# Kernel tuning notes

Hardware: AMD Instinct MI355X
Metric: run time of the kernel (lower is better)

## Reference

```python
import jax, jax.numpy as jnp
import numpy as np

H = 1024       # hidden_size
I = 1024       # intermediate_size
E = 16         # num_experts
K = 4          # experts_per_token
LIMIT = 7.0    # swiglu_limit
ALPHA = 1.702  # swiglu alpha
EPS = 1e-5     # rmsnorm eps


def setup_inputs() -> dict:
    key = jax.random.key(0)
    ks = jax.random.split(key, 8)
    x = jax.random.normal(ks[0], (2, 512, H), dtype=jnp.float32)
    norm_scale = jnp.ones((H,), dtype=jnp.float32)
    wg = jax.random.normal(ks[1], (H, E), dtype=jnp.float32) * 0.02
    bg = jax.random.normal(ks[2], (E,), dtype=jnp.float32) * 0.02
    w1 = jax.random.normal(ks[3], (E, H, 2 * I), dtype=jnp.float32) * 0.02
    b1 = jax.random.normal(ks[4], (E, 2 * I), dtype=jnp.float32) * 0.02
    w2 = jax.random.normal(ks[5], (E, I, H), dtype=jnp.float32) * 0.02
    b2 = jax.random.normal(ks[6], (E, H), dtype=jnp.float32) * 0.02
    return {"x": x, "norm_scale": norm_scale, "wg": wg, "bg": bg,
            "w1": w1, "b1": b1, "w2": w2, "b2": b2}


def reference(x, norm_scale, wg, bg, w1, b1, w2, b2):
    shape = x.shape
    xf = x.reshape(-1, shape[-1])                                   # [T, H]
    # RMSNorm (float32 math)
    xn = xf * jax.lax.rsqrt(jnp.mean(xf * xf, axis=-1, keepdims=True) + EPS) * norm_scale
    # router logits + top-k with softmax over selected logits
    logits = xn @ wg + bg                                           # [T, E]
    vals, idx = jax.lax.top_k(logits, K)                            # [T, K]
    gates = jax.nn.softmax(vals, axis=-1)                           # [T, K]
    # dense [T, E] gate matrix (exactly equivalent to gather/scatter grouped GEMM)
    gate_full = jnp.einsum('tke,tk->te', jax.nn.one_hot(idx, E, dtype=gates.dtype), gates)
    # expert FFN 1 + fused swiglu (interleaved gate/linear pairs)
    h = jnp.einsum('th,ehd->etd', xn, w1) + b1[:, None, :]          # [E, T, 2I]
    a = jnp.minimum(h[..., ::2], LIMIT)                             # gate branch
    b = jnp.clip(h[..., 1::2], -LIMIT, LIMIT)                       # linear branch
    s = a * jax.nn.sigmoid(ALPHA * a) * (b + 1.0)                   # [E, T, I]
    # expert FFN 2; gamma (gate) scales the full epilogue incl. bias
    y = jnp.einsum('eti,eih->eth', s, w2) + b2[:, None, :]          # [E, T, H]
    t = jnp.einsum('eth,te->th', y, gate_full)                      # scatter-combine
    return x + t.reshape(shape)
```

## Files before the change

kernel.cpp:

```cpp
#include <hip/hip_runtime.h>

#define NH 1024
#define NI2 2048
#define NI 1024
#define NE 16
#define NT 1024

static constexpr float LIMITF = 7.0f;
static constexpr float ALPHAF = 1.702f;
static constexpr float EPSF = 1e-5f;

typedef short bf16x8 __attribute__((ext_vector_type(8)));
typedef float f32x16 __attribute__((ext_vector_type(16)));

__device__ __forceinline__ unsigned short f2bf(float f) {
  unsigned int u = __builtin_bit_cast(unsigned int, f);
  u = (u + 0x7FFFu + ((u >> 16) & 1u)) >> 16;
  return (unsigned short)u;
}

__global__ __launch_bounds__(256) void k_init(const float* __restrict__ x,
                                              float* __restrict__ out) {
  int i = blockIdx.x * 256 + threadIdx.x;
  reinterpret_cast<float4*>(out)[i] = reinterpret_cast<const float4*>(x)[i];
}

__global__ __launch_bounds__(256) void k_norm_router(
    const float* __restrict__ x, const float* __restrict__ nsc,
    const float* __restrict__ wg, const float* __restrict__ bg,
    unsigned short* __restrict__ xn, int* __restrict__ topk_idx,
    float* __restrict__ topk_gate, int* __restrict__ counts) {
  int t = blockIdx.x;
  int tid = threadIdx.x;
  int wave = tid >> 6, lane = tid & 63;

  float4 v = reinterpret_cast<const float4*>(x + (size_t)t * NH)[tid];
  float ss = v.x * v.x + v.y * v.y + v.z * v.z + v.w * v.w;
  for (int off = 32; off; off >>= 1) ss += __shfl_xor(ss, off);

  __shared__ float red[4];
  __shared__ float redl[4][16];
  __shared__ float logits_s[16];
  if (lane == 0) red[wave] = ss;
  __syncthreads();
  float tot = red[0] + red[1] + red[2] + red[3];
  float r = rsqrtf(tot * (1.0f / NH) + EPSF);

  float4 sc = reinterpret_cast<const float4*>(nsc)[tid];
  float xv[4];
  xv[0] = v.x * r * sc.x;
  xv[1] = v.y * r * sc.y;
  xv[2] = v.z * r * sc.z;
  xv[3] = v.w * r * sc.w;

  ushort4 o;
  o.x = f2bf(xv[0]); o.y = f2bf(xv[1]); o.z = f2bf(xv[2]); o.w = f2bf(xv[3]);
  reinterpret_cast<ushort4*>(xn + (size_t)t * NH)[tid] = o;

  float acc[16];
#pragma unroll
  for (int e = 0; e < 16; e++) acc[e] = 0.f;
  int hbase = tid * 4;
#pragma unroll
  for (int i = 0; i < 4; i++) {
    const float4* wr = reinterpret_cast<const float4*>(wg + (size_t)(hbase + i) * NE);
#pragma unroll
    for (int j = 0; j < 4; j++) {
      float4 w = wr[j];
      acc[j * 4 + 0] += xv[i] * w.x;
      acc[j * 4 + 1] += xv[i] * w.y;
      acc[j * 4 + 2] += xv[i] * w.z;
      acc[j * 4 + 3] += xv[i] * w.w;
    }
  }
#pragma unroll
  for (int e = 0; e < 16; e++)
    for (int off = 32; off; off >>= 1) acc[e] += __shfl_xor(acc[e], off);
  if (lane == 0) {
#pragma unroll
    for (int e = 0; e < 16; e++) redl[wave][e] = acc[e];
  }
  __syncthreads();
  if (tid < 16)
    logits_s[tid] = redl[0][tid] + redl[1][tid] + redl[2][tid] + redl[3][tid] + bg[tid];
  __syncthreads();

  if (tid == 0) {
    float vals[16];
#pragma unroll
    for (int e = 0; e < 16; e++) vals[e] = logits_s[e];
    int sel[4]; float sv[4];
    unsigned used = 0;
    for (int k = 0; k < 4; k++) {
      float best = -1e30f; int bi = 0;
      for (int e = 0; e < 16; e++) {
        if (!((used >> e) & 1u) && vals[e] > best) { best = vals[e]; bi = e; }
      }
      used |= 1u << bi; sel[k] = bi; sv[k] = best;
    }
    float g[4], ssum = 0.f;
    for (int k = 0; k < 4; k++) { g[k] = __expf(sv[k] - sv[0]); ssum += g[k]; }
    for (int k = 0; k < 4; k++) {
      topk_idx[t * 4 + k] = sel[k];
      topk_gate[t * 4 + k] = g[k] / ssum;
      atomicAdd(&counts[sel[k]], 1);
    }
  }
}

__global__ void k_scan(const int* __restrict__ counts, int* __restrict__ offsets,
                       int* __restrict__ cursor) {
  if (blockIdx.x == 0 && threadIdx.x == 0) {
    int o = 0;
    for (int e = 0; e < NE; e++) { offsets[e] = o; cursor[e] = o; o += counts[e]; }
  }
}

__global__ __launch_bounds__(256) void k_fill(const int* __restrict__ topk_idx,
                                              const float* __restrict__ topk_gate,
                                              int* __restrict__ cursor,
                                              int* __restrict__ rows_tok,
                                              float* __restrict__ rows_gate) {
  int idx = blockIdx.x * 256 + threadIdx.x;
  if (idx >= NT * 4) return;
  int e = topk_idx[idx];
  int slot = atomicAdd(&cursor[e], 1);
  rows_tok[slot] = idx >> 2;
  rows_gate[slot] = topk_gate[idx];
}

__global__ __launch_bounds__(256) void k_ffn1(
    const unsigned short* __restrict__ xn, const float* __restrict__ w1,
    const float* __restrict__ b1, const int* __restrict__ counts,
    const int* __restrict__ offsets, const int* __restrict__ rows_tok,
    unsigned short* __restrict__ s_buf) {
  int e = blockIdx.y;
  int cnt = counts[e];
  if (cnt == 0) return;
  int n0 = blockIdx.x * 32;
  int rowbase = offsets[e];
  int tid = threadIdx.x;

  __shared__ __align__(16) unsigned short lds_b[128 * 32 * 8];

  const float* w1e = w1 + (size_t)e * (NH * NI2) + n0;
  {
    int col = tid & 31;
    int kc8 = tid >> 5;
    for (int p = 0; p < 16; p++) {
      int kb = p * 64 + kc8 * 8;
      float f[8];
#pragma unroll
      for (int j = 0; j < 8; j++) f[j] = w1e[(size_t)(kb + j) * NI2 + col];
      unsigned int pk[4];
#pragma unroll
      for (int j = 0; j < 4; j++)
        pk[j] = (unsigned)f2bf(f[2 * j]) | ((unsigned)f2bf(f[2 * j + 1]) << 16);
      *reinterpret_cast<uint4*>(&lds_b[(size_t)((kb >> 3) * 32 + col) * 8]) =
          *reinterpret_cast<const uint4*>(pk);
    }
  }
  __syncthreads();

  int lane = tid & 63;
  int wave = tid >> 6;
  int lrow = lane & 31;
  int khalf = lane >> 5;

  float bias = b1[(size_t)e * NI2 + n0 + lrow];
  int parity = lrow & 1;

  for (int m0 = 0; m0 < cnt; m0 += 256) {
    int tb0 = m0 + wave * 32;
    int tb1 = m0 + 128 + wave * 32;
    int tok0 = rows_tok[rowbase + min(tb0 + lrow, cnt - 1)];
    const unsigned short* a0p = xn + (size_t)tok0 * NH + khalf * 8;

    f32x16 acc0 = {0.f,0.f,0.f,0.f,0.f,0.f,0.f,0.f,0.f,0.f,0.f,0.f,0.f,0.f,0.f,0.f};
    f32x16 acc1 = {0.f,0.f,0.f,0.f,0.f,0.f,0.f,0.f,0.f,0.f,0.f,0.f,0.f,0.f,0.f,0.f};
    bool dual = (m0 + 128) < cnt;

    if (dual) {
      int tok1 = rows_tok[rowbase + min(tb1 + lrow, cnt - 1)];
      const unsigned short* a1p = xn + (size_t)tok1 * NH + khalf * 8;
#pragma unroll 4
      for (int k2 = 0; k2 < 64; k2++) {
        bf16x8 av0 = *reinterpret_cast<const bf16x8*>(a0p + k2 * 16);
        bf16x8 av1 = *reinterpret_cast<const bf16x8*>(a1p + k2 * 16);
        bf16x8 bv = *reinterpret_cast<const bf16x8*>(
            &lds_b[(size_t)((k2 * 2 + khalf) * 32 + lrow) * 8]);
        acc0 = __builtin_amdgcn_mfma_f32_32x32x16_bf16(av0, bv, acc0, 0, 0, 0);
        acc1 = __builtin_amdgcn_mfma_f32_32x32x16_bf16(av1, bv, acc1, 0, 0, 0);
      }
    } else {
#pragma unroll 4
      for (int k2 = 0; k2 < 64; k2++) {
        bf16x8 av0 = *reinterpret_cast<const bf16x8*>(a0p + k2 * 16);
        bf16x8 bv = *reinterpret_cast<const bf16x8*>(
            &lds_b[(size_t)((k2 * 2 + khalf) * 32 + lrow) * 8]);
        acc0 = __builtin_amdgcn_mfma_f32_32x32x16_bf16(av0, bv, acc0, 0, 0, 0);
      }
    }

#pragma unroll
    for (int t2 = 0; t2 < 2; t2++) {
      if (t2 == 1 && !dual) break;
      f32x16 acc = t2 ? acc1 : acc0;
      int tb = t2 ? tb1 : tb0;
#pragma unroll
      for (int reg = 0; reg < 16; reg++) {
        float v = acc[reg] + bias;
        float p = __shfl_xor(v, 1);
        int row = (reg & 3) + 8 * (reg >> 2) + 4 * khalf;
        int m = tb + row;
        if (!parity && m < cnt) {
          float aa = fminf(v, LIMITF);
          float bb = fminf(fmaxf(p, -LIMITF), LIMITF);
          float sig = 1.0f / (1.0f + __expf(-ALPHAF * aa));
          float sval = aa * sig * (bb + 1.0f);
          s_buf[(size_t)(rowbase + m) * NI + ((n0 + lrow) >> 1)] = f2bf(sval);
        }
      }
    }
  }
}

__global__ __launch_bounds__(256) void k_ffn2(
    const unsigned short* __restrict__ s_buf, const float* __restrict__ w2,
    const float* __restrict__ b2, const int* __restrict__ counts,
    const int* __restrict__ offsets, const int* __restrict__ rows_tok,
    const float* __restrict__ rows_gate, float* __restrict__ out) {
  int e = blockIdx.y;
  int cnt = counts[e];
  if (cnt == 0) return;
  int n0 = blockIdx.x * 32;
  int rowbase = offsets[e];
  int tid = threadIdx.x;

  __shared__ __align__(16) unsigned short lds_b[128 * 32 * 8];

  const float* w2e = w2 + (size_t)e * (NI * NH) + n0;
  {
    int col = tid & 31;
    int kc8 = tid >> 5;
    for (int p = 0; p < 16; p++) {
      int kb = p * 64 + kc8 * 8;
      float f[8];
#pragma unroll
      for (int j = 0; j < 8; j++) f[j] = w2e[(size_t)(kb + j) * NH + col];
      unsigned int pk[4];
#pragma unroll
      for (int j = 0; j < 4; j++)
        pk[j] = (unsigned)f2bf(f[2 * j]) | ((unsigned)f2bf(f[2 * j + 1]) << 16);
      *reinterpret_cast<uint4*>(&lds_b[(size_t)((kb >> 3) * 32 + col) * 8]) =
          *reinterpret_cast<const uint4*>(pk);
    }
  }
  __syncthreads();

  int lane = tid & 63;
  int wave = tid >> 6;
  int lrow = lane & 31;
  int khalf = lane >> 5;

  float b2v = b2[(size_t)e * NH + n0 + lrow];

  for (int m0 = 0; m0 < cnt; m0 += 256) {
    int tb0 = m0 + wave * 32;
    int tb1 = m0 + 128 + wave * 32;
    int r0 = rowbase + min(tb0 + lrow, cnt - 1);
    const unsigned short* a0p = s_buf + (size_t)r0 * NI + khalf * 8;

    f32x16 acc0 = {0.f,0.f,0.f,0.f,0.f,0.f,0.f,0.f,0.f,0.f,0.f,0.f,0.f,0.f,0.f,0.f};
    f32x16 acc1 = {0.f,0.f,0.f,0.f,0.f,0.f,0.f,0.f,0.f,0.f,0.f,0.f,0.f,0.f,0.f,0.f};
    bool dual = (m0 + 128) < cnt;

    if (dual) {
      int r1 = rowbase + min(tb1 + lrow, cnt - 1);
      const unsigned short* a1p = s_buf + (size_t)r1 * NI + khalf * 8;
#pragma unroll 4
      for (int k2 = 0; k2 < 64; k2++) {
        bf16x8 av0 = *reinterpret_cast<const bf16x8*>(a0p + k2 * 16);
        bf16x8 av1 = *reinterpret_cast<const bf16x8*>(a1p + k2 * 16);
        bf16x8 bv = *reinterpret_cast<const bf16x8*>(
            &lds_b[(size_t)((k2 * 2 + khalf) * 32 + lrow) * 8]);
        acc0 = __builtin_amdgcn_mfma_f32_32x32x16_bf16(av0, bv, acc0, 0, 0, 0);
        acc1 = __builtin_amdgcn_mfma_f32_32x32x16_bf16(av1, bv, acc1, 0, 0, 0);
      }
    } else {
#pragma unroll 4
      for (int k2 = 0; k2 < 64; k2++) {
        bf16x8 av0 = *reinterpret_cast<const bf16x8*>(a0p + k2 * 16);
        bf16x8 bv = *reinterpret_cast<const bf16x8*>(
            &lds_b[(size_t)((k2 * 2 + khalf) * 32 + lrow) * 8]);
        acc0 = __builtin_amdgcn_mfma_f32_32x32x16_bf16(av0, bv, acc0, 0, 0, 0);
      }
    }

#pragma unroll
    for (int t2 = 0; t2 < 2; t2++) {
      if (t2 == 1 && !dual) break;
      f32x16 acc = t2 ? acc1 : acc0;
      int tb = t2 ? tb1 : tb0;
#pragma unroll
      for (int reg = 0; reg < 16; reg++) {
        int row = (reg & 3) + 8 * (reg >> 2) + 4 * khalf;
        int m = tb + row;
        if (m < cnt) {
          int rr = rowbase + m;
          int tok = rows_tok[rr];
          float g = rows_gate[rr];
          atomicAdd(&out[(size_t)tok * NH + n0 + lrow], g * (acc[reg] + b2v));
        }
      }
    }
  }
}

extern "C" void kernel_launch(void* const* d_in, const int* in_sizes, int n_in,
                              void* d_out, int out_size, void* d_ws, size_t ws_size,
                              hipStream_t stream) {
  const float* x   = (const float*)d_in[0];
  const float* nsc = (const float*)d_in[1];
  const float* wg  = (const float*)d_in[2];
  const float* bg  = (const float*)d_in[3];
  const float* w1  = (const float*)d_in[4];
  const float* b1  = (const float*)d_in[5];
  const float* w2  = (const float*)d_in[6];
  const float* b2  = (const float*)d_in[7];
  float* out = (float*)d_out;
  char* ws = (char*)d_ws;

  int*   counts    = (int*)(ws + 0);
  int*   offsets   = (int*)(ws + 64);
  int*   cursor    = (int*)(ws + 128);
  int*   topk_idx  = (int*)(ws + 1024);
  float* topk_gate = (float*)(ws + 1024 + 16384);
  int*   rows_tok  = (int*)(ws + 1024 + 32768);
  float* rows_gate = (float*)(ws + 1024 + 49152);
  unsigned short* xn    = (unsigned short*)(ws + 131072);
  unsigned short* s_buf = (unsigned short*)(ws + 4 * 1024 * 1024);

  hipMemsetAsync(ws, 0, 256, stream);
  k_init<<<NT * NH / 1024, 256, 0, stream>>>(x, out);
  k_norm_router<<<NT, 256, 0, stream>>>(x, nsc, wg, bg, xn, topk_idx, topk_gate,
                                        counts);
  k_scan<<<1, 64, 0, stream>>>(counts, offsets, cursor);
  k_fill<<<16, 256, 0, stream>>>(topk_idx, topk_gate, cursor, rows_tok, rows_gate);
  k_ffn1<<<dim3(NI2 / 32, NE), 256, 0, stream>>>(xn, w1, b1, counts, offsets,
                                                 rows_tok, s_buf);
  k_ffn2<<<dim3(NH / 32, NE), 256, 0, stream>>>(s_buf, w2, b2, counts, offsets,
                                                rows_tok, rows_gate, out);
}
```

Before: 453.3 us.

## Double-buffer streamed weight tiles in FFN kernels and split-K FFN2

Replaces the upfront full-K weight load into 64KB LDS with a double-buffered stream of 128-row K chunks, prefetching the next chunk into registers while MFMAs consume the current one. The smaller LDS footprint plus launch bounds allows higher occupancy. FFN2 additionally splits K across two blocks accumulating via atomics, with bias added once. Weights are reloaded per M-tile when an expert exceeds 256 rows, and split-K doubles the atomic traffic on the output.

Measured after the change: 472.6 us. 4.2% more time.

```diff
diff --git a/kernel.cpp b/kernel.cpp
--- a/kernel.cpp
+++ b/kernel.cpp
@@ -129,7 +129,7 @@
   rows_gate[slot] = topk_gate[idx];
 }
 
-__global__ __launch_bounds__(256) void k_ffn1(
+__global__ __launch_bounds__(256, 4) void k_ffn1(
     const unsigned short* __restrict__ xn, const float* __restrict__ w1,
     const float* __restrict__ b1, const int* __restrict__ counts,
     const int* __restrict__ offsets, const int* __restrict__ rows_tok,
@@ -141,64 +141,90 @@
   int rowbase = offsets[e];
   int tid = threadIdx.x;
 
-  __shared__ __align__(16) unsigned short lds_b[128 * 32 * 8];
+  __shared__ __align__(16) unsigned short lds_b[2 * 16 * 32 * 8];
 
   const float* w1e = w1 + (size_t)e * (NH * NI2) + n0;
-  {
-    int col = tid & 31;
-    int kc8 = tid >> 5;
-    for (int p = 0; p < 16; p++) {
-      int kb = p * 64 + kc8 * 8;
-      float f[8];
-#pragma unroll
-      for (int j = 0; j < 8; j++) f[j] = w1e[(size_t)(kb + j) * NI2 + col];
-      unsigned int pk[4];
-#pragma unroll
-      for (int j = 0; j < 4; j++)
-        pk[j] = (unsigned)f2bf(f[2 * j]) | ((unsigned)f2bf(f[2 * j + 1]) << 16);
-      *reinterpret_cast<uint4*>(&lds_b[(size_t)((kb >> 3) * 32 + col) * 8]) =
-          *reinterpret_cast<const uint4*>(pk);
-    }
-  }
-  __syncthreads();
-
-  int lane = tid & 63;
-  int wave = tid >> 6;
-  int lrow = lane & 31;
-  int khalf = lane >> 5;
-
+  int col = tid & 31, kc8 = tid >> 5;
+
+  int lane = tid & 63, wave = tid >> 6;
+  int lrow = lane & 31, khalf = lane >> 5;
   float bias = b1[(size_t)e * NI2 + n0 + lrow];
   int parity = lrow & 1;
 
   for (int m0 = 0; m0 < cnt; m0 += 256) {
     int tb0 = m0 + wave * 32;
     int tb1 = m0 + 128 + wave * 32;
+    bool dual = (m0 + 128) < cnt;
     int tok0 = rows_tok[rowbase + min(tb0 + lrow, cnt - 1)];
-    const unsigned short* a0p = xn + (size_t)tok0 * NH + khalf * 8;
+    const unsigned short* a0p = xn + (size_t)tok0 * NH;
+    const unsigned short* a1p = a0p;
+    if (dual) {
+      int tok1 = rows_tok[rowbase + min(tb1 + lrow, cnt - 1)];
+      a1p = xn + (size_t)tok1 * NH;
+    }
 
     f32x16 acc0 = {0.f,0.f,0.f,0.f,0.f,0.f,0.f,0.f,0.f,0.f,0.f,0.f,0.f,0.f,0.f,0.f};
     f32x16 acc1 = {0.f,0.f,0.f,0.f,0.f,0.f,0.f,0.f,0.f,0.f,0.f,0.f,0.f,0.f,0.f,0.f};
-    bool dual = (m0 + 128) < cnt;
-
-    if (dual) {
-      int tok1 = rows_tok[rowbase + min(tb1 + lrow, cnt - 1)];
-      const unsigned short* a1p = xn + (size_t)tok1 * NH + khalf * 8;
-#pragma unroll 4
-      for (int k2 = 0; k2 < 64; k2++) {
-        bf16x8 av0 = *reinterpret_cast<const bf16x8*>(a0p + k2 * 16);
-        bf16x8 av1 = *reinterpret_cast<const bf16x8*>(a1p + k2 * 16);
+
+    __syncthreads();
+#pragma unroll
+    for (int half = 0; half < 2; half++) {
+      int kcz = kc8 + half * 8;
+      int kb = kcz * 8;
+      float f[8];
+#pragma unroll
+      for (int j = 0; j < 8; j++) f[j] = w1e[(size_t)(kb + j) * NI2 + col];
+      unsigned pk[4];
+#pragma unroll
+      for (int j = 0; j < 4; j++)
+        pk[j] = (unsigned)f2bf(f[2 * j]) | ((unsigned)f2bf(f[2 * j + 1]) << 16);
+      *reinterpret_cast<uint4*>(&lds_b[(size_t)(kcz * 32 + col) * 8]) =
+          *reinterpret_cast<const uint4*>(pk);
+    }
+    __syncthreads();
+
+    int buf = 0;
+    for (int kt = 0; kt < 8; kt++) {
+      float fst[2][8];
+      if (kt < 7) {
+        int k0n = (kt + 1) * 128;
+#pragma unroll
+        for (int half = 0; half < 2; half++) {
+          int kb = (kc8 + half * 8) * 8;
+#pragma unroll
+          for (int j = 0; j < 8; j++)
+            fst[half][j] = w1e[(size_t)(k0n + kb + j) * NI2 + col];
+        }
+      }
+      const unsigned short* ab0 = a0p + kt * 128 + khalf * 8;
+      const unsigned short* ab1 = a1p + kt * 128 + khalf * 8;
+#pragma unroll
+      for (int k2 = 0; k2 < 8; k2++) {
         bf16x8 bv = *reinterpret_cast<const bf16x8*>(
-            &lds_b[(size_t)((k2 * 2 + khalf) * 32 + lrow) * 8]);
+            &lds_b[(size_t)(((buf * 16) + k2 * 2 + khalf) * 32 + lrow) * 8]);
+        bf16x8 av0 = *reinterpret_cast<const bf16x8*>(ab0 + k2 * 16);
         acc0 = __builtin_amdgcn_mfma_f32_32x32x16_bf16(av0, bv, acc0, 0, 0, 0);
-        acc1 = __builtin_amdgcn_mfma_f32_32x32x16_bf16(av1, bv, acc1, 0, 0, 0);
-      }
-    } else {
-#pragma unroll 4
-      for (int k2 = 0; k2 < 64; k2++) {
-        bf16x8 av0 = *reinterpret_cast<const bf16x8*>(a0p + k2 * 16);
-        bf16x8 bv = *reinterpret_cast<const bf16x8*>(
-            &lds_b[(size_t)((k2 * 2 + khalf) * 32 + lrow) * 8]);
-        acc0 = __builtin_amdgcn_mfma_f32_32x32x16_bf16(av0, bv, acc0, 0, 0, 0);
+        if (dual) {
+          bf16x8 av1 = *reinterpret_cast<const bf16x8*>(ab1 + k2 * 16);
+          acc1 = __builtin_amdgcn_mfma_f32_32x32x16_bf16(av1, bv, acc1, 0, 0, 0);
+        }
+      }
+      if (kt < 7) {
+        int nb = buf ^ 1;
+#pragma unroll
+        for (int half = 0; half < 2; half++) {
+          int kcz = kc8 + half * 8;
+          unsigned pk[4];
+#pragma unroll
+          for (int j = 0; j < 4; j++)
+            pk[j] = (unsigned)f2bf(fst[half][2 * j]) |
+                    ((unsigned)f2bf(fst[half][2 * j + 1]) << 16);
+          *reinterpret_cast<uint4*>(
+              &lds_b[(size_t)((nb * 16 + kcz) * 32 + col) * 8]) =
+              *reinterpret_cast<const uint4*>(pk);
+        }
+        __syncthreads();
+        buf = nb;
       }
     }
 
@@ -225,7 +251,7 @@
   }
 }
 
-__global__ __launch_bounds__(256) void k_ffn2(
+__global__ __launch_bounds__(256, 4) void k_ffn2(
     const unsigned short* __restrict__ s_buf, const float* __restrict__ w2,
     const float* __restrict__ b2, const int* __restrict__ counts,
     const int* __restrict__ offsets, const int* __restrict__ rows_tok,
@@ -234,66 +260,95 @@
   int cnt = counts[e];
   if (cnt == 0) return;
   int n0 = blockIdx.x * 32;
+  int ks = blockIdx.z;
   int rowbase = offsets[e];
   int tid = threadIdx.x;
 
-  __shared__ __align__(16) unsigned short lds_b[128 * 32 * 8];
+  __shared__ __align__(16) unsigned short lds_b[2 * 16 * 32 * 8];
 
   const float* w2e = w2 + (size_t)e * (NI * NH) + n0;
-  {
-    int col = tid & 31;
-    int kc8 = tid >> 5;
-    for (int p = 0; p < 16; p++) {
-      int kb = p * 64 + kc8 * 8;
-      float f[8];
-#pragma unroll
-      for (int j = 0; j < 8; j++) f[j] = w2e[(size_t)(kb + j) * NH + col];
-      unsigned int pk[4];
-#pragma unroll
-      for (int j = 0; j < 4; j++)
-        pk[j] = (unsigned)f2bf(f[2 * j]) | ((unsigned)f2bf(f[2 * j + 1]) << 16);
-      *reinterpret_cast<uint4*>(&lds_b[(size_t)((kb >> 3) * 32 + col) * 8]) =
-          *reinterpret_cast<const uint4*>(pk);
-    }
-  }
-  __syncthreads();
-
-  int lane = tid & 63;
-  int wave = tid >> 6;
-  int lrow = lane & 31;
-  int khalf = lane >> 5;
-
-  float b2v = b2[(size_t)e * NH + n0 + lrow];
+  int col = tid & 31, kc8 = tid >> 5;
+  int kbase = ks * 512;
+
+  int lane = tid & 63, wave = tid >> 6;
+  int lrow = lane & 31, khalf = lane >> 5;
+  float b2v = (ks == 0) ? b2[(size_t)e * NH + n0 + lrow] : 0.f;
 
   for (int m0 = 0; m0 < cnt; m0 += 256) {
     int tb0 = m0 + wave * 32;
     int tb1 = m0 + 128 + wave * 32;
+    bool dual = (m0 + 128) < cnt;
     int r0 = rowbase + min(tb0 + lrow, cnt - 1);
-    const unsigned short* a0p = s_buf + (size_t)r0 * NI + khalf * 8;
+    const unsigned short* a0p = s_buf + (size_t)r0 * NI + kbase;
+    const unsigned short* a1p = a0p;
+    if (dual) {
+      int r1 = rowbase + min(tb1 + lrow, cnt - 1);
+      a1p = s_buf + (size_t)r1 * NI + kbase;
+    }
 
     f32x16 acc0 = {0.f,0.f,0.f,0.f,0.f,0.f,0.f,0.f,0.f,0.f,0.f,0.f,0.f,0.f,0.f,0.f};
     f32x16 acc1 = {0.f,0.f,0.f,0.f,0.f,0.f,0.f,0.f,0.f,0.f,0.f,0.f,0.f,0.f,0.f,0.f};
-    bool dual = (m0 + 128) < cnt;
-
-    if (dual) {
-      int r1 = rowbase + min(tb1 + lrow, cnt - 1);
-      const unsigned short* a1p = s_buf + (size_t)r1 * NI + khalf * 8;
-#pragma unroll 4
-      for (int k2 = 0; k2 < 64; k2++) {
-        bf16x8 av0 = *reinterpret_cast<const bf16x8*>(a0p + k2 * 16);
-        bf16x8 av1 = *reinterpret_cast<const bf16x8*>(a1p + k2 * 16);
+
+    __syncthreads();
+#pragma unroll
+    for (int half = 0; half < 2; half++) {
+      int kcz = kc8 + half * 8;
+      int kb = kcz * 8;
+      float f[8];
+#pragma unroll
+      for (int j = 0; j < 8; j++)
+        f[j] = w2e[(size_t)(kbase + kb + j) * NH + col];
+      unsigned pk[4];
+#pragma unroll
+      for (int j = 0; j < 4; j++)
+        pk[j] = (unsigned)f2bf(f[2 * j]) | ((unsigned)f2bf(f[2 * j + 1]) << 16);
+      *reinterpret_cast<uint4*>(&lds_b[(size_t)(kcz * 32 + col) * 8]) =
+          *reinterpret_cast<const uint4*>(pk);
+    }
+    __syncthreads();
+
+    int buf = 0;
+    for (int kt = 0; kt < 4; kt++) {
+      float fst[2][8];
+      if (kt < 3) {
+        int k0n = kbase + (kt + 1) * 128;
+#pragma unroll
+        for (int half = 0; half < 2; half++) {
+          int kb = (kc8 + half * 8) * 8;
+#pragma unroll
+          for (int j = 0; j < 8; j++)
+            fst[half][j] = w2e[(size_t)(k0n + kb + j) * NH + col];
+        }
+      }
+      const unsigned short* ab0 = a0p + kt * 128 + khalf * 8;
+      const unsigned short* ab1 = a1p + kt * 128 + khalf * 8;
+#pragma unroll
+      for (int k2 = 0; k2 < 8; k2++) {
         bf16x8 bv = *reinterpret_cast<const bf16x8*>(
-            &lds_b[(size_t)((k2 * 2 + khalf) * 32 + lrow) * 8]);
+            &lds_b[(size_t)(((buf * 16) + k2 * 2 + khalf) * 32 + lrow) * 8]);
+        bf16x8 av0 = *reinterpret_cast<const bf16x8*>(ab0 + k2 * 16);
         acc0 = __builtin_amdgcn_mfma_f32_32x32x16_bf16(av0, bv, acc0, 0, 0, 0);
-        acc1 = __builtin_amdgcn_mfma_f32_32x32x16_bf16(av1, bv, acc1, 0, 0, 0);
-      }
-    } else {
-#pragma unroll 4
-      for (int k2 = 0; k2 < 64; k2++) {
-        bf16x8 av0 = *reinterpret_cast<const bf16x8*>(a0p + k2 * 16);
-        bf16x8 bv = *reinterpret_cast<const bf16x8*>(
-            &lds_b[(size_t)((k2 * 2 + khalf) * 32 + lrow) * 8]);
-        acc0 = __builtin_amdgcn_mfma_f32_32x32x16_bf16(av0, bv, acc0, 0, 0, 0);
+        if (dual) {
+          bf16x8 av1 = *reinterpret_cast<const bf16x8*>(ab1 + k2 * 16);
+          acc1 = __builtin_amdgcn_mfma_f32_32x32x16_bf16(av1, bv, acc1, 0, 0, 0);
+        }
+      }
+      if (kt < 3) {
+        int nb = buf ^ 1;
+#pragma unroll
+        for (int half = 0; half < 2; half++) {
+          int kcz = kc8 + half * 8;
+          unsigned pk[4];
+#pragma unroll
+          for (int j = 0; j < 4; j++)
+            pk[j] = (unsigned)f2bf(fst[half][2 * j]) |
+                    ((unsigned)f2bf(fst[half][2 * j + 1]) << 16);
+          *reinterpret_cast<uint4*>(
+              &lds_b[(size_t)((nb * 16 + kcz) * 32 + col) * 8]) =
+              *reinterpret_cast<const uint4*>(pk);
+        }
+        __syncthreads();
+        buf = nb;
       }
     }
 
@@ -349,6 +404,6 @@
   k_fill<<<16, 256, 0, stream>>>(topk_idx, topk_gate, cursor, rows_tok, rows_gate);
   k_ffn1<<<dim3(NI2 / 32, NE), 256, 0, stream>>>(xn, w1, b1, counts, offsets,
                                                  rows_tok, s_buf);
-  k_ffn2<<<dim3(NH / 32, NE), 256, 0, stream>>>(s_buf, w2, b2, counts, offsets,
-                                                rows_tok, rows_gate, out);
-}
+  k_ffn2<<<dim3(NH / 32, NE, 2), 256, 0, stream>>>(s_buf, w2, b2, counts, offsets,
+                                                   rows_tok, rows_gate, out);
+}
```
